# Performance work log

Measured on AMD Instinct MI355X. Metric: run time of the kernel, lower is better.

## Reference

```python
import math
import jax, jax.numpy as jnp
import numpy as np

N_HEAD = 16
ROPE_BASE = 10000.0


def _rope_tables(T, half, dtype):
    # build_sin_cos(seq_len, dim=head_dim//2): inv freq of length `half`
    pos = jnp.arange(T, dtype=jnp.float32)[:, None]                       # (T,1)
    inv = jnp.exp(jnp.arange(0, 2 * half, 2, dtype=jnp.float32) * (-math.log(ROPE_BASE) / (2 * half)))
    ang = pos * inv                                                        # (T, half)
    return jnp.sin(ang).astype(dtype), jnp.cos(ang).astype(dtype)


def _apply_rope(q, k, sin, cos):
    # q,k: (B,T,H,Dh); sin,cos: (T, Dh//2) -> broadcast over batch and heads
    half = q.shape[-1] // 2
    s = sin[None, :, None, :]
    c = cos[None, :, None, :]
    q1, q2 = q[..., :half], q[..., half:]
    k1, k2 = k[..., :half], k[..., half:]
    q = jnp.concatenate([q1 * c - q2 * s, q2 * c + q1 * s], axis=-1)
    k = jnp.concatenate([k1 * c - k2 * s, k2 * c + k1 * s], axis=-1)
    return q, k


def setup_inputs() -> dict:
    key = jax.random.key(0)
    k1, k2, k3 = jax.random.split(key, 3)
    B, T, C = 2, 2048, 2048
    x = jax.random.normal(k1, (B, T, C), dtype=jnp.float32)
    w_qkv = jax.random.normal(k2, (3 * C, C), dtype=jnp.float32) * (1.0 / math.sqrt(C))
    w_proj = jax.random.normal(k3, (C, C), dtype=jnp.float32) * (1.0 / math.sqrt(C))
    return {"x": x, "w_qkv": w_qkv, "w_proj": w_proj}


def reference(x, w_qkv, w_proj):
    B, T, C = x.shape
    H = N_HEAD
    Dh = C // H
    # fused QKV projection (Linear, no bias): (B,T,3C) -> (B,T,3,H,Dh)
    qkv = jnp.einsum('btc,oc->bto', x, w_qkv).reshape(B, T, 3, H, Dh)
    q, k, v = qkv[:, :, 0], qkv[:, :, 1], qkv[:, :, 2]          # (B,T,H,Dh)
    sin, cos = _rope_tables(T, Dh // 2, x.dtype)
    q, k = _apply_rope(q, k, sin, cos)
    # causal attention, scale 1/sqrt(Dh) (flash default softmax_scale=None)
    scale = 1.0 / math.sqrt(Dh)
    scores = jnp.einsum('bqhd,bkhd->bhqk', q, k) * scale        # (B,H,T,T)
    mask = jnp.tril(jnp.ones((T, T), dtype=bool))
    scores = jnp.where(mask[None, None], scores, jnp.finfo(scores.dtype).min)
    probs = jax.nn.softmax(scores, axis=-1)
    out = jnp.einsum('bhqk,bkhd->bqhd', probs, v)               # (B,T,H,Dh)
    # faithful to original: permute(0,2,1,3) then reshape_as(x)
    out = jnp.transpose(out, (0, 2, 1, 3)).reshape(B, T, C)
    return jnp.einsum('btc,oc->bto', out, w_proj)
```

## Files before the change

kernel.cpp:

```cpp
#include <hip/hip_runtime.h>
#include <hip/hip_bf16.h>

typedef __bf16 bf16_t;
typedef __bf16 bf16x8 __attribute__((ext_vector_type(8)));
typedef __bf16 bf16x4 __attribute__((ext_vector_type(4)));
typedef float f32x4 __attribute__((ext_vector_type(4)));
typedef float f32x16 __attribute__((ext_vector_type(16)));
typedef unsigned u32x4v __attribute__((ext_vector_type(4)));

#define MFMA16(a, b, c) __builtin_amdgcn_mfma_f32_16x16x32_bf16(a, b, c, 0, 0, 0)
#define MFMA32(a, b, c) __builtin_amdgcn_mfma_f32_32x32x16_bf16(a, b, c, 0, 0, 0)

__device__ __forceinline__ void async_copy16(const void* g, void* l) {
  __builtin_amdgcn_global_load_lds(
      (const __attribute__((address_space(1))) void*)g,
      (__attribute__((address_space(3))) void*)l, 16, 0, 0);
}

__device__ __forceinline__ unsigned cvtpk(float lo, float hi) {
  unsigned r;
  asm("v_cvt_pk_bf16_f32 %0, %1, %2" : "=v"(r) : "v"(lo), "v"(hi));
  return r;
}

__global__ void cast_all(const float* __restrict__ x, const float* __restrict__ wqkv,
                         const float* __restrict__ wproj, bf16_t* __restrict__ xb,
                         bf16_t* __restrict__ wqkvb, bf16_t* __restrict__ wprojb) {
  int stride = gridDim.x * blockDim.x;
  for (int i = blockIdx.x * blockDim.x + threadIdx.x; i < 3145728; i += stride) {
    const float* src;
    bf16_t* dst;
    int idx;
    if (i < 1048576) { src = x; dst = xb; idx = i; }
    else if (i < 2621440) { src = wqkv; dst = wqkvb; idx = i - 1048576; }
    else { src = wproj; dst = wprojb; idx = i - 2621440; }
    const float* p = src + (size_t)idx * 8;
    f32x4 a = *(const f32x4*)p;
    f32x4 b = *(const f32x4*)(p + 4);
    bf16x8 o;
    o[0] = (bf16_t)a[0]; o[1] = (bf16_t)a[1]; o[2] = (bf16_t)a[2]; o[3] = (bf16_t)a[3];
    o[4] = (bf16_t)b[0]; o[5] = (bf16_t)b[1]; o[6] = (bf16_t)b[2]; o[7] = (bf16_t)b[3];
    *(bf16x8*)(dst + (size_t)idx * 8) = o;
  }
}

__global__ __launch_bounds__(512, 2) void gemm_qkv(
    const bf16_t* __restrict__ A, const bf16_t* __restrict__ Bw,
    bf16_t* __restrict__ qo, bf16_t* __restrict__ ko,
    int K) {
  __shared__ __align__(16) char lds[131072];
  int tid = threadIdx.x;
  int w = tid >> 6, lane = tid & 63;
  int wm = w & 1, wn = w >> 1;
  int mr = lane & 15, kg = lane >> 4;

  int orig = blockIdx.x;
  int chunk = orig & 7, i = orig >> 3;
  int by = (chunk & 3) * 4 + (i & 3);
  int bx = (chunk >> 2) * 8 + (i >> 2);
  int row0 = by * 256, col0 = bx * 256;

  int lr = tid >> 3, ch = (tid & 7) ^ (lr & 7);
  size_t aoff[4], boff[4];
#pragma unroll
  for (int g = 0; g < 4; ++g) {
    int gr = g * 32 + (lr & 31) + (lr >> 5) * 128;
    aoff[g] = (size_t)(row0 + gr) * K + ch * 8;
  }
#pragma unroll
  for (int p = 0; p < 4; ++p) {
    int gr = (lr >> 4) * 64 + p * 16 + (lr & 15);
    boff[p] = (size_t)(col0 + gr) * K + ch * 8;
  }

  auto stgA = [&](int q, int g, int kt) {
    async_copy16(A + aoff[g] + kt * 64, lds + q * 65536 + g * 8192 + tid * 16);
  };
  auto stgB = [&](int q, int p, int kt) {
    async_copy16(Bw + boff[p] + kt * 64, lds + q * 65536 + 32768 + p * 8192 + tid * 16);
  };

  f32x4 zero = {0.f, 0.f, 0.f, 0.f};
  f32x4 acc[8][4];
#pragma unroll
  for (int mi = 0; mi < 8; ++mi)
#pragma unroll
    for (int ni = 0; ni < 4; ++ni) acc[mi][ni] = zero;

  int nt = K >> 6;

  stgB(0, 0, 0); stgB(0, 1, 0); stgB(0, 2, 0); stgB(0, 3, 0);
  stgA(0, 0, 0); stgA(0, 1, 0); stgA(0, 2, 0); stgA(0, 3, 0);
  asm volatile("s_waitcnt vmcnt(0)" ::: "memory");
  __builtin_amdgcn_sched_barrier(0);
  __builtin_amdgcn_s_barrier();
  __builtin_amdgcn_sched_barrier(0);

#pragma unroll 1
  for (int t = 0; t < nt; ++t) {
    int q = t & 1, qn = q ^ 1;
    int kt = (t + 1 < nt) ? (t + 1) : t;
    const char* Ab = lds + q * 65536;
    const char* Bb = Ab + 32768;
    bf16x8 bf[4][2];

#define QKV_PHASE(MI0, STG, DOWAIT)                                             \
    {                                                                           \
      int r0 = ((MI0) >> 1) * 64 + wm * 32 + mr;                                \
      int r1 = r0 + 16;                                                         \
      bf16x8 a00 = *(const bf16x8*)(Ab + r0 * 128 + ((kg * 16) ^ ((r0 & 7) << 4)));      \
      bf16x8 a01 = *(const bf16x8*)(Ab + r0 * 128 + ((64 + kg * 16) ^ ((r0 & 7) << 4))); \
      bf16x8 a10 = *(const bf16x8*)(Ab + r1 * 128 + ((kg * 16) ^ ((r1 & 7) << 4)));      \
      bf16x8 a11 = *(const bf16x8*)(Ab + r1 * 128 + ((64 + kg * 16) ^ ((r1 & 7) << 4))); \
      STG;                                                                      \
      __builtin_amdgcn_sched_barrier(0);                                        \
      if (DOWAIT) { asm volatile("s_waitcnt vmcnt(4)" ::: "memory"); }          \
      __builtin_amdgcn_s_barrier();                                             \
      asm volatile("s_waitcnt lgkmcnt(0)" ::: "memory");                        \
      __builtin_amdgcn_sched_barrier(0);                                        \
      __builtin_amdgcn_s_setprio(1);                                            \
      _Pragma("unroll")                                                         \
      for (int ni = 0; ni < 4; ++ni) {                                          \
        acc[MI0][ni] = MFMA16(a00, bf[ni][0], acc[MI0][ni]);                    \
        acc[MI0][ni] = MFMA16(a01, bf[ni][1], acc[MI0][ni]);                    \
        acc[(MI0) + 1][ni] = MFMA16(a10, bf[ni][0], acc[(MI0) + 1][ni]);        \
        acc[(MI0) + 1][ni] = MFMA16(a11, bf[ni][1], acc[(MI0) + 1][ni]);        \
      }                                                                         \
      __builtin_amdgcn_s_setprio(0);                                            \
      __builtin_amdgcn_sched_barrier(0);                                        \
      __builtin_amdgcn_s_barrier();                                             \
      __builtin_amdgcn_sched_barrier(0);                                        \
    }

#pragma unroll
    for (int ni = 0; ni < 4; ++ni) {
      int rb = ni * 64 + wn * 16 + mr;
      bf[ni][0] = *(const bf16x8*)(Bb + rb * 128 + ((kg * 16) ^ ((rb & 7) << 4)));
      bf[ni][1] = *(const bf16x8*)(Bb + rb * 128 + ((64 + kg * 16) ^ ((rb & 7) << 4)));
    }
    QKV_PHASE(0, (stgA(qn, 0, kt), stgA(qn, 1, kt), stgB(qn, 0, kt), stgB(qn, 1, kt)), 1)
    QKV_PHASE(2, (stgA(qn, 2, kt), stgA(qn, 3, kt), stgB(qn, 2, kt), stgB(qn, 3, kt)), 0)
    QKV_PHASE(4, (void)0, 0)
    QKV_PHASE(6, (void)0, 0)
#undef QKV_PHASE
  }
  asm volatile("s_waitcnt vmcnt(0)" ::: "memory");
  __syncthreads();

  char* tb = &lds[0];
  int s = col0 >> 11;
  int h0 = (col0 >> 7) & 15;
  int b = row0 >> 11, t0 = row0 & 2047;
#pragma unroll
  for (int mi = 0; mi < 8; ++mi)
#pragma unroll
    for (int ni = 0; ni < 4; ++ni)
#pragma unroll
      for (int jj = 0; jj < 4; ++jj) {
        int rl = wm * 128 + mi * 16 + kg * 4 + jj;
        int cb = (wn * 64 + ni * 16 + mr) * 2;
        *(bf16_t*)(tb + rl * 512 + (cb ^ ((rl & 7) << 4))) = (bf16_t)acc[mi][ni][jj];
      }
  __syncthreads();
  int r = tid >> 1, hs = tid & 1;
  const char* rowb = tb + r * 512;
  int sz = (r & 7) << 4;
  int t = t0 + r;
  bf16_t* dst = (s == 0 ? qo : ko) + ((size_t)((b * 16 + h0 + hs) * 2048 + t)) * 128;
  float tf = (float)t;
  const float cinv = -0.20762050593046014f;
  float postm = (s == 0) ? 0.12751744f : 1.0f;
  bf16x8 vin[16];
#pragma unroll
  for (int m = 0; m < 16; ++m)
    vin[m] = *(const bf16x8*)(rowb + ((hs * 256 + m * 16) ^ sz));
#pragma unroll
  for (int m = 0; m < 8; ++m) {
    bf16x8 o1, o2;
#pragma unroll
    for (int e = 0; e < 8; ++e) {
      float ang = tf * exp2f((float)(m * 8 + e) * cinv);
      float sv = __sinf(ang), cv = __cosf(ang);
      float x1 = (float)vin[m][e], x2 = (float)vin[m + 8][e];
      o1[e] = (bf16_t)((x1 * cv - x2 * sv) * postm);
      o2[e] = (bf16_t)((x2 * cv + x1 * sv) * postm);
    }
    *(bf16x8*)(dst + m * 8) = o1;
    *(bf16x8*)(dst + 64 + m * 8) = o2;
  }
}

template <int MODE>
__global__ __launch_bounds__(512, 2) void gemm256(
    const bf16_t* __restrict__ A, const bf16_t* __restrict__ Bw, float* __restrict__ C,
    bf16_t* __restrict__ vto, int M, int N, int K, int nby, int colbase) {
  __shared__ __align__(16) char lds[147456];
  int tid = threadIdx.x;
  int w = tid >> 6, lane = tid & 63;
  int wm = w >> 1, wn = w & 1;
  int mr = lane & 15, kg = lane >> 4;

  int nwg = gridDim.x;
  int orig = blockIdx.x;
  int wgid = (orig & 7) * (nwg >> 3) + (orig >> 3);
  int by = wgid % nby, bx = wgid / nby;
  int row0 = by * 256, col0 = colbase + bx * 128;

  size_t aoff[4], boff[2];
#pragma unroll
  for (int it = 0; it < 4; ++it) {
    int c = tid + it * 512;
    int r = c >> 3;
    int chs = (c & 7) ^ (r & 7);
    aoff[it] = (size_t)(row0 + r) * K + chs * 8;
  }
#pragma unroll
  for (int it = 0; it < 2; ++it) {
    int c = tid + it * 512;
    int r = c >> 3;
    int chs = (c & 7) ^ (r & 7);
    boff[it] = (size_t)(col0 - colbase + r) * K + chs * 8;
  }

  auto stageA = [&](int buf, int kt, int half) {
    char* Ad = &lds[buf * 49152];
#pragma unroll
    for (int it = half * 2; it < half * 2 + 2; ++it)
      async_copy16(A + aoff[it] + kt * 64, Ad + (tid + it * 512) * 16);
  };
  auto stageB = [&](int buf, int kt) {
    char* Bd = &lds[buf * 49152 + 32768];
#pragma unroll
    for (int it = 0; it < 2; ++it)
      async_copy16(Bw + boff[it] + kt * 64, Bd + (tid + it * 512) * 16);
  };

  f32x4 zero = {0.f, 0.f, 0.f, 0.f};
  f32x4 acc[4][4];
#pragma unroll
  for (int mi = 0; mi < 4; ++mi)
#pragma unroll
    for (int ni = 0; ni < 4; ++ni) acc[mi][ni] = zero;

  int nt = K >> 6;
  stageA(0, 0, 0); stageA(0, 0, 1); stageB(0, 0);
  stageA(1, 1, 0); stageA(1, 1, 1); stageB(1, 1);
  asm volatile("s_waitcnt vmcnt(6)" ::: "memory");
  __builtin_amdgcn_sched_barrier(0);
  __builtin_amdgcn_s_barrier();
  __builtin_amdgcn_sched_barrier(0);

#pragma unroll 1
  for (int t = 0; t < nt; ++t) {
    int cur = t % 3;
    int nxt = (t + 2) % 3;
    int kt2 = (t + 2 < nt) ? (t + 2) : t;
    const char* Ab = &lds[cur * 49152];
    const char* Bb = &lds[cur * 49152 + 32768];
    bf16x8 af[4][2], bfr[4][2];
#pragma unroll
    for (int mi = 0; mi < 4; ++mi) {
      int row = wm * 64 + mi * 16 + mr;
      const char* rb = Ab + row * 128;
      int sz = (row & 7) << 4;
      af[mi][0] = *(const bf16x8*)(rb + ((kg * 16) ^ sz));
      af[mi][1] = *(const bf16x8*)(rb + ((64 + kg * 16) ^ sz));
    }
#pragma unroll
    for (int ni = 0; ni < 4; ++ni) {
      int row = wn * 64 + ni * 16 + mr;
      const char* rb = Bb + row * 128;
      int sz = (row & 7) << 4;
      bfr[ni][0] = *(const bf16x8*)(rb + ((kg * 16) ^ sz));
      bfr[ni][1] = *(const bf16x8*)(rb + ((64 + kg * 16) ^ sz));
    }
    stageA(nxt, kt2, 0);
    __builtin_amdgcn_s_setprio(1);
#pragma unroll
    for (int mi = 0; mi < 4; ++mi) {
      acc[mi][0] = MFMA16(af[mi][0], bfr[0][0], acc[mi][0]);
      acc[mi][0] = MFMA16(af[mi][1], bfr[0][1], acc[mi][0]);
    }
    __builtin_amdgcn_s_setprio(0);
    stageA(nxt, kt2, 1);
    __builtin_amdgcn_s_setprio(1);
#pragma unroll
    for (int mi = 0; mi < 4; ++mi) {
      acc[mi][1] = MFMA16(af[mi][0], bfr[1][0], acc[mi][1]);
      acc[mi][1] = MFMA16(af[mi][1], bfr[1][1], acc[mi][1]);
    }
    __builtin_amdgcn_s_setprio(0);
    stageB(nxt, kt2);
    __builtin_amdgcn_s_setprio(1);
#pragma unroll
    for (int mi = 0; mi < 4; ++mi) {
      acc[mi][2] = MFMA16(af[mi][0], bfr[2][0], acc[mi][2]);
      acc[mi][2] = MFMA16(af[mi][1], bfr[2][1], acc[mi][2]);
      acc[mi][3] = MFMA16(af[mi][0], bfr[3][0], acc[mi][3]);
      acc[mi][3] = MFMA16(af[mi][1], bfr[3][1], acc[mi][3]);
    }
    __builtin_amdgcn_s_setprio(0);
    asm volatile("s_waitcnt vmcnt(6)" ::: "memory");
    __builtin_amdgcn_sched_barrier(0);
    __builtin_amdgcn_s_barrier();
    __builtin_amdgcn_sched_barrier(0);
  }
  asm volatile("s_waitcnt vmcnt(0)" ::: "memory");
  __syncthreads();

  if (MODE == 0) {
#pragma unroll
    for (int mi = 0; mi < 4; ++mi)
#pragma unroll
      for (int ni = 0; ni < 4; ++ni)
#pragma unroll
        for (int jj = 0; jj < 4; ++jj) {
          int row = row0 + wm * 64 + mi * 16 + kg * 4 + jj;
          int col = col0 + wn * 64 + ni * 16 + mr;
          C[(size_t)row * N + col] = acc[mi][ni][jj];
        }
  } else {
    char* tb = &lds[0];
    int h = (col0 >> 7) & 15;
    int b = row0 >> 11, t0 = row0 & 2047;
#pragma unroll
    for (int mi = 0; mi < 4; ++mi)
#pragma unroll
      for (int ni = 0; ni < 4; ++ni)
#pragma unroll
        for (int jj = 0; jj < 4; ++jj) {
          int rloc = wm * 64 + mi * 16 + kg * 4 + jj;
          int cloc = wn * 64 + ni * 16 + mr;
          *(bf16_t*)(tb + cloc * 512 + ((rloc * 2) ^ ((cloc & 7) << 4))) =
              (bf16_t)acc[mi][ni][jj];
        }
    __syncthreads();
    int d = tid >> 2, qt = tid & 3;
    const char* rowb = tb + d * 512;
    int sz = (d & 7) << 4;
    bf16_t* dst = vto + ((size_t)((b * 16 + h) * 128 + d)) * 2048 + t0 + qt * 64;
#pragma unroll
    for (int m2 = 0; m2 < 8; ++m2)
      *(bf16x8*)(dst + m2 * 8) = *(const bf16x8*)(rowb + ((qt * 128 + m2 * 16) ^ sz));
  }
}

__global__ __launch_bounds__(256, 2) void attn_kernel(
    const bf16_t* __restrict__ qg, const bf16_t* __restrict__ kgl,
    const bf16_t* __restrict__ vtg, bf16_t* __restrict__ og) {
  __shared__ __align__(16) bf16_t Ks[2][64 * 128];
  __shared__ __align__(16) bf16_t Vs[2][128 * 64];
  const int T = 2048;
  int tid = threadIdx.x;
  int w = tid >> 6, lane = tid & 63;
  int l31 = lane & 31, hi = lane >> 5;

  int L = blockIdx.x;
  int halfg = L >> 8;
  int Lr = L & 255;
  int role = (Lr & 7) * 32 + (Lr >> 3);
  int bx = role & 7, bh = role >> 3;
  int qb = halfg ? bx : (15 - bx);

  const bf16_t* Q = qg + (size_t)bh * T * 128;
  const bf16_t* K = kgl + (size_t)bh * T * 128;
  const bf16_t* Vt = vtg + (size_t)bh * 128 * T;

  int sb = tid * 16;
  int krl = sb >> 8;
  int kc = (sb & 255) ^ (krl << 4);
  size_t ksrc = (size_t)krl * 128 + (kc >> 1);
  int vdl = sb >> 7;
  int vc = (sb & 127) ^ ((vdl & 7) << 4);
  size_t vsrc = (size_t)vdl * 2048 + (vc >> 1);

  auto stage = [&](int buf, int kb) {
#pragma unroll
    for (int it = 0; it < 4; ++it)
      async_copy16(K + (size_t)(kb + it * 16) * 128 + ksrc, &Ks[buf][it * 2048 + tid * 8]);
#pragma unroll
    for (int it = 0; it < 4; ++it)
      async_copy16(Vt + (size_t)it * 65536 + kb + vsrc, &Vs[buf][it * 2048 + tid * 8]);
  };

  int b = bh >> 4, h = bh & 15;
  f32x16 zero16 = {0.f};
  int swzK = (l31 & 15) << 4;
  int swzV = (l31 & 7) << 4;

  int qw0 = qb * 128 + w * 32;
  int tq = qw0 + l31;
  const bf16_t* qrow = Q + (size_t)tq * 128 + hi * 8;
  bf16x8 qf[8];
#pragma unroll
  for (int dc = 0; dc < 8; ++dc) qf[dc] = *(const bf16x8*)(qrow + dc * 16);

  f32x16 acc[4];
#pragma unroll
  for (int dt = 0; dt < 4; ++dt) acc[dt] = zero16;
  float mrun = -1e30f, lpart = 0.f;

  int nj = 2 * qb + 2;
  stage(0, 0);
  stage(1, 64);
#pragma unroll 1
  for (int j = 0; j < nj; ++j) {
    int cur = j & 1;
    if (j + 1 < nj) {
      asm volatile("s_waitcnt vmcnt(8)" ::: "memory");
    } else {
      asm volatile("s_waitcnt vmcnt(0)" ::: "memory");
    }
    __builtin_amdgcn_sched_barrier(0);
    __syncthreads();
    int kb = j * 64;
    if (kb <= qw0) {
      const char* KsB = (const char*)&Ks[cur][0];
      const char* VsB = (const char*)&Vs[cur][0];
      f32x16 s0 = zero16, s1 = zero16;
      __builtin_amdgcn_s_setprio(1);
#pragma unroll
      for (int dc = 0; dc < 8; ++dc) {
        int cb = dc * 32 + hi * 16;
        bf16x8 k0 = *(const bf16x8*)(KsB + l31 * 256 + (cb ^ swzK));
        bf16x8 k1 = *(const bf16x8*)(KsB + (32 + l31) * 256 + (cb ^ swzK));
        s0 = MFMA32(k0, qf[dc], s0);
        s1 = MFMA32(k1, qf[dc], s1);
      }
      __builtin_amdgcn_s_setprio(0);
      float p0[16], p1[16];
      float lmax = -3e38f;
      bool diag = (kb + 63 > qw0);
#pragma unroll
      for (int r = 0; r < 16; ++r) {
        int kk = (r & 3) + 8 * (r >> 2) + 4 * hi;
        float v0 = s0[r], v1 = s1[r];
        if (diag) {
          if (kb + kk > tq) v0 = -1e30f;
          if (kb + 32 + kk > tq) v1 = -1e30f;
        }
        p0[r] = v0; p1[r] = v1;
        lmax = fmaxf(lmax, fmaxf(v0, v1));
      }
      bool ok = (lmax <= mrun + 8.0f);
      if (!__all(ok)) {
        float tmax = fmaxf(lmax, __shfl_xor(lmax, 32, 64));
        float mn = fmaxf(mrun, tmax);
        float corr = __builtin_amdgcn_exp2f(mrun - mn);
        mrun = mn;
        lpart *= corr;
#pragma unroll
        for (int dt = 0; dt < 4; ++dt)
#pragma unroll
          for (int r = 0; r < 16; ++r) acc[dt][r] *= corr;
      }
#pragma unroll
      for (int r = 0; r < 16; ++r) {
        float e0 = __builtin_amdgcn_exp2f(p0[r] - mrun);
        float e1 = __builtin_amdgcn_exp2f(p1[r] - mrun);
        p0[r] = e0; p1[r] = e1;
        lpart += e0 + e1;
      }
      bf16x8 pa0, pa1, pa2, pa3;
#define BUILD_PA(dst, P, B0)                                         \
      { unsigned a0 = cvtpk(P[(B0) + 0], P[(B0) + 1]);               \
        unsigned a1 = cvtpk(P[(B0) + 2], P[(B0) + 3]);               \
        unsigned b0 = cvtpk(P[(B0) + 4], P[(B0) + 5]);               \
        unsigned b1 = cvtpk(P[(B0) + 6], P[(B0) + 7]);               \
        unsigned xa0 = __shfl_xor(a0, 32, 64);                       \
        unsigned xa1 = __shfl_xor(a1, 32, 64);                       \
        unsigned xb0 = __shfl_xor(b0, 32, 64);                       \
        unsigned xb1 = __shfl_xor(b1, 32, 64);                       \
        u32x4v fw;                                                   \
        fw[0] = hi ? xb0 : a0; fw[1] = hi ? xb1 : a1;                \
        fw[2] = hi ? b0 : xa0; fw[3] = hi ? b1 : xa1;                \
        dst = __builtin_bit_cast(bf16x8, fw); }
      BUILD_PA(pa0, p0, 0)
      BUILD_PA(pa1, p0, 8)
      BUILD_PA(pa2, p1, 0)
      BUILD_PA(pa3, p1, 8)
#undef BUILD_PA
      __builtin_amdgcn_s_setprio(1);
#pragma unroll
      for (int dt = 0; dt < 4; ++dt) {
        const char* vrow = VsB + (dt * 32 + l31) * 128;
        bf16x8 v0 = *(const bf16x8*)(vrow + ((hi * 16) ^ swzV));
        bf16x8 v1 = *(const bf16x8*)(vrow + ((32 + hi * 16) ^ swzV));
        bf16x8 v2 = *(const bf16x8*)(vrow + ((64 + hi * 16) ^ swzV));
        bf16x8 v3 = *(const bf16x8*)(vrow + ((96 + hi * 16) ^ swzV));
        acc[dt] = MFMA32(v0, pa0, acc[dt]);
        acc[dt] = MFMA32(v1, pa1, acc[dt]);
        acc[dt] = MFMA32(v2, pa2, acc[dt]);
        acc[dt] = MFMA32(v3, pa3, acc[dt]);
      }
      __builtin_amdgcn_s_setprio(0);
    }
    __syncthreads();
    if (j + 2 < nj) stage(cur, (j + 2) * 64);
  }
  float l = lpart + __shfl_xor(lpart, 32, 64);
  float invl = 1.0f / l;
  size_t orow_idx = (size_t)b * 2048 + h * 128 + (tq >> 4);
  bf16_t* orow = og + orow_idx * 2048 + (tq & 15) * 128;
#pragma unroll
  for (int dt = 0; dt < 4; ++dt)
#pragma unroll
    for (int g = 0; g < 4; ++g) {
      bf16x4 v4;
#pragma unroll
      for (int e = 0; e < 4; ++e) v4[e] = (bf16_t)(acc[dt][4 * g + e] * invl);
      *(bf16x4*)(orow + dt * 32 + 8 * g + 4 * hi) = v4;
    }
}

extern "C" void kernel_launch(void* const* d_in, const int* in_sizes, int n_in,
                              void* d_out, int out_size, void* d_ws, size_t ws_size,
                              hipStream_t stream) {
  const float* x = (const float*)d_in[0];
  const float* wqkv = (const float*)d_in[1];
  const float* wproj = (const float*)d_in[2];
  float* out = (float*)d_out;
  char* ws = (char*)d_ws;

  const size_t OFF_WQKV = 16777216;
  const size_t OFF_WPROJ = 41943040;
  const size_t OFF_Q = 50331648;
  const size_t OFF_K = 67108864;
  const size_t OFF_VT = 83886080;

  bf16_t* xb = (bf16_t*)(ws);
  bf16_t* wqkvb = (bf16_t*)(ws + OFF_WQKV);
  bf16_t* wprojb = (bf16_t*)(ws + OFF_WPROJ);
  bf16_t* g_q = (bf16_t*)(ws + OFF_Q);
  bf16_t* g_k = (bf16_t*)(ws + OFF_K);
  bf16_t* g_vt = (bf16_t*)(ws + OFF_VT);
  bf16_t* g_att = (bf16_t*)(ws);

  cast_all<<<4096, 256, 0, stream>>>(x, wqkv, wproj, xb, wqkvb, wprojb);
  gemm_qkv<<<256, 512, 0, stream>>>(xb, wqkvb, g_q, g_k, 2048);
  gemm256<1><<<256, 512, 0, stream>>>(xb, wqkvb + (size_t)4096 * 2048, nullptr, g_vt,
                                      4096, 2048, 2048, 16, 4096);
  attn_kernel<<<512, 256, 0, stream>>>(g_q, g_k, g_vt, g_att);
  gemm256<0><<<256, 512, 0, stream>>>(g_att, wprojb, out, nullptr, 4096, 2048, 2048, 16, 0);
}
```

Measured before the change: 243.3 us.

## Restructure attention to single-wave blocks loading K/V directly into registers

Replaces the 4-wave, 128-query attention block with a one-wave, 32-query block that reads K and V tiles straight from global memory into registers, dropping LDS staging, double buffering and block barriers. Key tiles shrink to 32 and the grid grows to 2048 blocks, with a new XCD-aware mapping and exact causal trip counts. Running-sum accumulators are split to shorten dependency chains. The cost is that K/V are no longer shared across waves in LDS, so global and L2 traffic rise, and loads are not explicitly prefetched ahead of use.

```diff
diff --git a/kernel.cpp b/kernel.cpp
--- a/kernel.cpp
+++ b/kernel.cpp
@@ -345,159 +345,123 @@
   }
 }
 
-__global__ __launch_bounds__(256, 2) void attn_kernel(
+__global__ __launch_bounds__(64, 2) void attn_kernel(
     const bf16_t* __restrict__ qg, const bf16_t* __restrict__ kgl,
     const bf16_t* __restrict__ vtg, bf16_t* __restrict__ og) {
-  __shared__ __align__(16) bf16_t Ks[2][64 * 128];
-  __shared__ __align__(16) bf16_t Vs[2][128 * 64];
   const int T = 2048;
-  int tid = threadIdx.x;
-  int w = tid >> 6, lane = tid & 63;
+  int lane = threadIdx.x;
   int l31 = lane & 31, hi = lane >> 5;
 
   int L = blockIdx.x;
-  int halfg = L >> 8;
-  int Lr = L & 255;
-  int role = (Lr & 7) * 32 + (Lr >> 3);
-  int bx = role & 7, bh = role >> 3;
-  int qb = halfg ? bx : (15 - bx);
+  int xcd = L & 7, rest = L >> 3;
+  int bh = xcd * 4 + (rest & 3);
+  int qc = 63 - (rest >> 2);
 
   const bf16_t* Q = qg + (size_t)bh * T * 128;
   const bf16_t* K = kgl + (size_t)bh * T * 128;
   const bf16_t* Vt = vtg + (size_t)bh * 128 * T;
 
-  int sb = tid * 16;
-  int krl = sb >> 8;
-  int kc = (sb & 255) ^ (krl << 4);
-  size_t ksrc = (size_t)krl * 128 + (kc >> 1);
-  int vdl = sb >> 7;
-  int vc = (sb & 127) ^ ((vdl & 7) << 4);
-  size_t vsrc = (size_t)vdl * 2048 + (vc >> 1);
-
-  auto stage = [&](int buf, int kb) {
-#pragma unroll
-    for (int it = 0; it < 4; ++it)
-      async_copy16(K + (size_t)(kb + it * 16) * 128 + ksrc, &Ks[buf][it * 2048 + tid * 8]);
-#pragma unroll
-    for (int it = 0; it < 4; ++it)
-      async_copy16(Vt + (size_t)it * 65536 + kb + vsrc, &Vs[buf][it * 2048 + tid * 8]);
-  };
-
+  int qw0 = qc * 32;
+  int tq = qw0 + l31;
   int b = bh >> 4, h = bh & 15;
-  f32x16 zero16 = {0.f};
-  int swzK = (l31 & 15) << 4;
-  int swzV = (l31 & 7) << 4;
-
-  int qw0 = qb * 128 + w * 32;
-  int tq = qw0 + l31;
+
   const bf16_t* qrow = Q + (size_t)tq * 128 + hi * 8;
   bf16x8 qf[8];
 #pragma unroll
   for (int dc = 0; dc < 8; ++dc) qf[dc] = *(const bf16x8*)(qrow + dc * 16);
 
+  f32x16 zero16 = {0.f};
   f32x16 acc[4];
 #pragma unroll
   for (int dt = 0; dt < 4; ++dt) acc[dt] = zero16;
-  float mrun = -1e30f, lpart = 0.f;
-
-  int nj = 2 * qb + 2;
-  stage(0, 0);
-  stage(1, 64);
+  float mrun = -1e30f, lpa = 0.f, lpb = 0.f;
+
+  const bf16_t* Kb = K + (size_t)l31 * 128 + hi * 8;
+  const bf16_t* Vb = Vt + (size_t)l31 * 2048 + hi * 8;
+
+  int nj = qc + 1;
 #pragma unroll 1
   for (int j = 0; j < nj; ++j) {
-    int cur = j & 1;
-    if (j + 1 < nj) {
-      asm volatile("s_waitcnt vmcnt(8)" ::: "memory");
-    } else {
-      asm volatile("s_waitcnt vmcnt(0)" ::: "memory");
-    }
-    __builtin_amdgcn_sched_barrier(0);
-    __syncthreads();
-    int kb = j * 64;
-    if (kb <= qw0) {
-      const char* KsB = (const char*)&Ks[cur][0];
-      const char* VsB = (const char*)&Vs[cur][0];
-      f32x16 s0 = zero16, s1 = zero16;
-      __builtin_amdgcn_s_setprio(1);
-#pragma unroll
-      for (int dc = 0; dc < 8; ++dc) {
-        int cb = dc * 32 + hi * 16;
-        bf16x8 k0 = *(const bf16x8*)(KsB + l31 * 256 + (cb ^ swzK));
-        bf16x8 k1 = *(const bf16x8*)(KsB + (32 + l31) * 256 + (cb ^ swzK));
-        s0 = MFMA32(k0, qf[dc], s0);
-        s1 = MFMA32(k1, qf[dc], s1);
-      }
-      __builtin_amdgcn_s_setprio(0);
-      float p0[16], p1[16];
-      float lmax = -3e38f;
-      bool diag = (kb + 63 > qw0);
+    int kb = j * 32;
+    bf16x8 kr[8];
+    const bf16_t* kp = Kb + (size_t)kb * 128;
+#pragma unroll
+    for (int dc = 0; dc < 8; ++dc) kr[dc] = *(const bf16x8*)(kp + dc * 16);
+    bf16x8 vr[8];
+#pragma unroll
+    for (int dt = 0; dt < 4; ++dt)
+#pragma unroll
+      for (int ks = 0; ks < 2; ++ks)
+        vr[dt * 2 + ks] = *(const bf16x8*)(Vb + (size_t)dt * 65536 + kb + ks * 16);
+    f32x16 s0 = zero16;
+    __builtin_amdgcn_s_setprio(1);
+#pragma unroll
+    for (int dc = 0; dc < 8; ++dc) s0 = MFMA32(kr[dc], qf[dc], s0);
+    __builtin_amdgcn_s_setprio(0);
+    float p0[16];
+    float lma = -3e38f, lmb = -3e38f;
+    if (j == qc) {
 #pragma unroll
       for (int r = 0; r < 16; ++r) {
         int kk = (r & 3) + 8 * (r >> 2) + 4 * hi;
-        float v0 = s0[r], v1 = s1[r];
-        if (diag) {
-          if (kb + kk > tq) v0 = -1e30f;
-          if (kb + 32 + kk > tq) v1 = -1e30f;
-        }
-        p0[r] = v0; p1[r] = v1;
-        lmax = fmaxf(lmax, fmaxf(v0, v1));
+        float v = s0[r];
+        if (kb + kk > tq) v = -1e30f;
+        p0[r] = v;
+        if (r & 1) lmb = fmaxf(lmb, v); else lma = fmaxf(lma, v);
       }
-      bool ok = (lmax <= mrun + 8.0f);
-      if (!__all(ok)) {
-        float tmax = fmaxf(lmax, __shfl_xor(lmax, 32, 64));
-        float mn = fmaxf(mrun, tmax);
-        float corr = __builtin_amdgcn_exp2f(mrun - mn);
-        mrun = mn;
-        lpart *= corr;
-#pragma unroll
-        for (int dt = 0; dt < 4; ++dt)
-#pragma unroll
-          for (int r = 0; r < 16; ++r) acc[dt][r] *= corr;
+    } else {
+#pragma unroll
+      for (int r = 0; r < 16; ++r) {
+        p0[r] = s0[r];
+        if (r & 1) lmb = fmaxf(lmb, s0[r]); else lma = fmaxf(lma, s0[r]);
       }
-#pragma unroll
-      for (int r = 0; r < 16; ++r) {
-        float e0 = __builtin_amdgcn_exp2f(p0[r] - mrun);
-        float e1 = __builtin_amdgcn_exp2f(p1[r] - mrun);
-        p0[r] = e0; p1[r] = e1;
-        lpart += e0 + e1;
-      }
-      bf16x8 pa0, pa1, pa2, pa3;
+    }
+    float lmax = fmaxf(lma, lmb);
+    bool ok = (lmax <= mrun + 8.0f);
+    if (!__all(ok)) {
+      float tmax = fmaxf(lmax, __shfl_xor(lmax, 32, 64));
+      float mn = fmaxf(mrun, tmax);
+      float corr = __builtin_amdgcn_exp2f(mrun - mn);
+      mrun = mn;
+      lpa *= corr;
+      lpb *= corr;
+#pragma unroll
+      for (int dt = 0; dt < 4; ++dt)
+#pragma unroll
+        for (int r = 0; r < 16; ++r) acc[dt][r] *= corr;
+    }
+#pragma unroll
+    for (int r = 0; r < 16; ++r) {
+      float e0 = __builtin_amdgcn_exp2f(p0[r] - mrun);
+      p0[r] = e0;
+      if (r & 1) lpb += e0; else lpa += e0;
+    }
+    bf16x8 pa0, pa1;
 #define BUILD_PA(dst, P, B0)                                         \
-      { unsigned a0 = cvtpk(P[(B0) + 0], P[(B0) + 1]);               \
-        unsigned a1 = cvtpk(P[(B0) + 2], P[(B0) + 3]);               \
-        unsigned b0 = cvtpk(P[(B0) + 4], P[(B0) + 5]);               \
-        unsigned b1 = cvtpk(P[(B0) + 6], P[(B0) + 7]);               \
-        unsigned xa0 = __shfl_xor(a0, 32, 64);                       \
-        unsigned xa1 = __shfl_xor(a1, 32, 64);                       \
-        unsigned xb0 = __shfl_xor(b0, 32, 64);                       \
-        unsigned xb1 = __shfl_xor(b1, 32, 64);                       \
-        u32x4v fw;                                                   \
-        fw[0] = hi ? xb0 : a0; fw[1] = hi ? xb1 : a1;                \
-        fw[2] = hi ? b0 : xa0; fw[3] = hi ? b1 : xa1;                \
-        dst = __builtin_bit_cast(bf16x8, fw); }
-      BUILD_PA(pa0, p0, 0)
-      BUILD_PA(pa1, p0, 8)
-      BUILD_PA(pa2, p1, 0)
-      BUILD_PA(pa3, p1, 8)
+    { unsigned a0 = cvtpk(P[(B0) + 0], P[(B0) + 1]);                 \
+      unsigned a1 = cvtpk(P[(B0) + 2], P[(B0) + 3]);                 \
+      unsigned b0 = cvtpk(P[(B0) + 4], P[(B0) + 5]);                 \
+      unsigned b1 = cvtpk(P[(B0) + 6], P[(B0) + 7]);                 \
+      unsigned xa0 = __shfl_xor(a0, 32, 64);                         \
+      unsigned xa1 = __shfl_xor(a1, 32, 64);                         \
+      unsigned xb0 = __shfl_xor(b0, 32, 64);                         \
+      unsigned xb1 = __shfl_xor(b1, 32, 64);                         \
+      u32x4v fw;                                                     \
+      fw[0] = hi ? xb0 : a0; fw[1] = hi ? xb1 : a1;                  \
+      fw[2] = hi ? b0 : xa0; fw[3] = hi ? b1 : xa1;                  \
+      dst = __builtin_bit_cast(bf16x8, fw); }
+    BUILD_PA(pa0, p0, 0)
+    BUILD_PA(pa1, p0, 8)
 #undef BUILD_PA
-      __builtin_amdgcn_s_setprio(1);
-#pragma unroll
-      for (int dt = 0; dt < 4; ++dt) {
-        const char* vrow = VsB + (dt * 32 + l31) * 128;
-        bf16x8 v0 = *(const bf16x8*)(vrow + ((hi * 16) ^ swzV));
-        bf16x8 v1 = *(const bf16x8*)(vrow + ((32 + hi * 16) ^ swzV));
-        bf16x8 v2 = *(const bf16x8*)(vrow + ((64 + hi * 16) ^ swzV));
-        bf16x8 v3 = *(const bf16x8*)(vrow + ((96 + hi * 16) ^ swzV));
-        acc[dt] = MFMA32(v0, pa0, acc[dt]);
-        acc[dt] = MFMA32(v1, pa1, acc[dt]);
-        acc[dt] = MFMA32(v2, pa2, acc[dt]);
-        acc[dt] = MFMA32(v3, pa3, acc[dt]);
-      }
-      __builtin_amdgcn_s_setprio(0);
-    }
-    __syncthreads();
-    if (j + 2 < nj) stage(cur, (j + 2) * 64);
-  }
+    __builtin_amdgcn_s_setprio(1);
+#pragma unroll
+    for (int dt = 0; dt < 4; ++dt) {
+      acc[dt] = MFMA32(vr[dt * 2], pa0, acc[dt]);
+      acc[dt] = MFMA32(vr[dt * 2 + 1], pa1, acc[dt]);
+    }
+    __builtin_amdgcn_s_setprio(0);
+  }
+  float lpart = lpa + lpb;
   float l = lpart + __shfl_xor(lpart, 32, 64);
   float invl = 1.0f / l;
   size_t orow_idx = (size_t)b * 2048 + h * 128 + (tq >> 4);
@@ -540,6 +504,6 @@
   gemm_qkv<<<256, 512, 0, stream>>>(xb, wqkvb, g_q, g_k, 2048);
   gemm256<1><<<256, 512, 0, stream>>>(xb, wqkvb + (size_t)4096 * 2048, nullptr, g_vt,
                                       4096, 2048, 2048, 16, 4096);
-  attn_kernel<<<512, 256, 0, stream>>>(g_q, g_k, g_vt, g_att);
+  attn_kernel<<<2048, 64, 0, stream>>>(g_q, g_k, g_vt, g_att);
   gemm256<0><<<256, 512, 0, stream>>>(g_att, wprojb, out, nullptr, 4096, 2048, 2048, 16, 0);
 }
```

After: 302.1 us. 24.2% more time.
